# Optimization experiments

Hardware: AMD Instinct MI355X
Metric: run time of the kernel (lower is better)

Reference implementation:

```python
import jax, jax.numpy as jnp
import numpy as np

EPS = 1e-5

def _round_ste(x):
    # straight-through round (identical value in fwd; STE grad in bwd module)
    return x + jax.lax.stop_gradient(jnp.round(x) - x)

def _quant_weight(w, bits):
    # per-tensor symmetric absmax quantization to `bits` bits (BitNet-style)
    qb = float(2 ** (bits - 1) - 1)
    scale = qb / jnp.maximum(jnp.max(jnp.abs(w)), EPS)
    return _round_ste(jnp.clip(w * scale, -qb, qb)) / scale

def _quant_act(x):
    # per-token 8-bit absmax activation quantization
    qb = 127.0
    scale = qb / jnp.maximum(jnp.max(jnp.abs(x), axis=-1, keepdims=True), EPS)
    return _round_ste(jnp.clip(x * scale, -qb, qb)) / scale

def _layernorm(x, gamma, beta):
    mu = jnp.mean(x, axis=-1, keepdims=True)
    var = jnp.mean(jnp.square(x - mu), axis=-1, keepdims=True)
    return (x - mu) * jax.lax.rsqrt(var + EPS) * gamma + beta

def _qlinear(x, w, b, bits):
    return jnp.einsum('btd,fd->btf', _quant_act(x), _quant_weight(w, bits)) + b

def setup_inputs() -> dict:
    key = jax.random.key(0)
    ks = jax.random.split(key, 4)
    B, T, D, F = 8, 2048, 1024, 4096
    return {
        'x': jax.random.normal(ks[0], (B, T, D), dtype=jnp.float32),
        'mask': jnp.ones((B, T, 1), dtype=jnp.float32),
        'ln_gamma': jnp.ones((D,), dtype=jnp.float32),
        'ln_beta': jnp.zeros((D,), dtype=jnp.float32),
        'w1': jax.random.normal(ks[1], (F, D), dtype=jnp.float32) * (1.0 / np.sqrt(D)),
        'b1': jnp.zeros((F,), dtype=jnp.float32),
        'w2': jax.random.normal(ks[2], (D, F), dtype=jnp.float32) * (1.0 / np.sqrt(F)),
        'b2': jnp.zeros((D,), dtype=jnp.float32),
        'bitwidth': 8,
    }

def reference(x, mask, ln_gamma, ln_beta, w1, b1, w2, b2, bitwidth):
    y = _layernorm(x, ln_gamma, ln_beta)           # [B,T,D]
    y = _qlinear(y, w1, b1, bitwidth)              # [B,T,F]
    y = y * jax.nn.sigmoid(y)                      # swish
    y = _qlinear(y, w2, b2, bitwidth)              # [B,T,D]
    seq_mask = mask[:, :, 0][..., None]            # [B,T,1]
    y = y * seq_mask
    return x + 0.5 * y
```

## Files before the change

kernel.cpp:

```cpp
#include <hip/hip_runtime.h>
#include <hip/hip_bf16.h>
#include <stdint.h>


typedef int v4i __attribute__((ext_vector_type(4)));
typedef int v16i __attribute__((ext_vector_type(16)));

__device__ __forceinline__ float wave_max64(float v) {
#pragma unroll
  for (int off = 32; off; off >>= 1) v = fmaxf(v, __shfl_xor(v, off, 64));
  return v;
}

__device__ __forceinline__ void load16_to_lds(const int8_t* g, int8_t* l) {
  __builtin_amdgcn_global_load_lds((const __attribute__((address_space(1))) void*)g,
                                   (__attribute__((address_space(3))) void*)l, 16, 0, 0);
}

__global__ __launch_bounds__(256) void absmax_kernel(const float* __restrict__ w, int n4,
                                                     int* __restrict__ slot) {
  float m = 0.f;
  const float4* w4 = (const float4*)w;
  for (int i = blockIdx.x * 256 + threadIdx.x; i < n4; i += gridDim.x * 256) {
    float4 v = w4[i];
    m = fmaxf(fmaxf(fabsf(v.x), fabsf(v.y)), fmaxf(fmaxf(fabsf(v.z), fabsf(v.w)), m));
  }
  m = wave_max64(m);
  __shared__ float sm[4];
  int lane = threadIdx.x & 63, wv = threadIdx.x >> 6;
  if (!lane) sm[wv] = m;
  __syncthreads();
  if (!threadIdx.x) {
    m = fmaxf(fmaxf(sm[0], sm[1]), fmaxf(sm[2], sm[3]));
    atomicMax(slot, __float_as_int(m));
  }
}

__global__ void scales_kernel(const int* __restrict__ wmax, const int* __restrict__ bits,
                              float* __restrict__ scal) {
  float qb = (float)((1 << (bits[0] - 1)) - 1);
  scal[2] = qb / fmaxf(__int_as_float(wmax[0]), 1e-5f);
  scal[3] = qb / fmaxf(__int_as_float(wmax[1]), 1e-5f);
  scal[4] = qb;
}

__global__ __launch_bounds__(256) void wquant_kernel(const float* __restrict__ w,
                                                     const float* __restrict__ scal, int which,
                                                     int8_t* __restrict__ out) {
  float s = scal[2 + which], qb = scal[4];
  int i = blockIdx.x * 256 + threadIdx.x;
  float4 v = ((const float4*)w)[i];
  char4 q;
  q.x = (char)(int)rintf(fminf(fmaxf(v.x * s, -qb), qb));
  q.y = (char)(int)rintf(fminf(fmaxf(v.y * s, -qb), qb));
  q.z = (char)(int)rintf(fminf(fmaxf(v.z * s, -qb), qb));
  q.w = (char)(int)rintf(fminf(fmaxf(v.w * s, -qb), qb));
  ((char4*)out)[i] = q;
}

__global__ __launch_bounds__(256) void ln_quant_kernel(const float* __restrict__ x,
                                                       const float* __restrict__ gamma,
                                                       const float* __restrict__ beta,
                                                       int8_t* __restrict__ xq,
                                                       float* __restrict__ xscale) {
  const int row = blockIdx.x;
  const int tid = threadIdx.x;
  const float4 v = ((const float4*)(x + (size_t)row * 1024))[tid];
  float s = v.x + v.y + v.z + v.w;
  float ss = fmaf(v.x, v.x, fmaf(v.y, v.y, fmaf(v.z, v.z, v.w * v.w)));
#pragma unroll
  for (int off = 32; off; off >>= 1) {
    s += __shfl_xor(s, off, 64);
    ss += __shfl_xor(ss, off, 64);
  }
  __shared__ float sm[8];
  const int lane = tid & 63, wv = tid >> 6;
  if (!lane) { sm[wv] = s; sm[4 + wv] = ss; }
  __syncthreads();
  s = sm[0] + sm[1] + sm[2] + sm[3];
  ss = sm[4] + sm[5] + sm[6] + sm[7];
  const float mu = s * (1.f / 1024.f);
  const float var = ss * (1.f / 1024.f) - mu * mu;
  const float rstd = rsqrtf(var + 1e-5f);
  const float4 g = ((const float4*)gamma)[tid];
  const float4 bb = ((const float4*)beta)[tid];
  float y0 = (v.x - mu) * rstd * g.x + bb.x;
  float y1 = (v.y - mu) * rstd * g.y + bb.y;
  float y2 = (v.z - mu) * rstd * g.z + bb.z;
  float y3 = (v.w - mu) * rstd * g.w + bb.w;
  float am = fmaxf(fmaxf(fabsf(y0), fabsf(y1)), fmaxf(fabsf(y2), fabsf(y3)));
  am = wave_max64(am);
  __syncthreads();
  if (!lane) sm[wv] = am;
  __syncthreads();
  am = fmaxf(fmaxf(sm[0], sm[1]), fmaxf(sm[2], sm[3]));
  const float scale = 127.f / fmaxf(am, 1e-5f);
  char4 q;
  q.x = (char)(int)rintf(fminf(fmaxf(y0 * scale, -127.f), 127.f));
  q.y = (char)(int)rintf(fminf(fmaxf(y1 * scale, -127.f), 127.f));
  q.z = (char)(int)rintf(fminf(fmaxf(y2 * scale, -127.f), 127.f));
  q.w = (char)(int)rintf(fminf(fmaxf(y3 * scale, -127.f), 127.f));
  ((char4*)(xq + (size_t)row * 1024))[tid] = q;
  if (!tid) xscale[row] = scale;
}

__global__ __launch_bounds__(256) void hquant_kernel(const ushort* __restrict__ h,
                                                     int8_t* __restrict__ hq,
                                                     float* __restrict__ hscale) {
  const int row = blockIdx.x;
  const int tid = threadIdx.x;
  const int4* p = (const int4*)(h + (size_t)row * 4096);
  union { int4 i4; ushort u[8]; } ua, ub;
  ua.i4 = p[tid * 2];
  ub.i4 = p[tid * 2 + 1];
  float f[16];
#pragma unroll
  for (int i = 0; i < 8; ++i) f[i] = __uint_as_float((unsigned)ua.u[i] << 16);
#pragma unroll
  for (int i = 0; i < 8; ++i) f[8 + i] = __uint_as_float((unsigned)ub.u[i] << 16);
  float am = 0.f;
#pragma unroll
  for (int i = 0; i < 16; ++i) am = fmaxf(am, fabsf(f[i]));
  am = wave_max64(am);
  __shared__ float sm[4];
  const int lane = tid & 63, wv = tid >> 6;
  if (!lane) sm[wv] = am;
  __syncthreads();
  am = fmaxf(fmaxf(sm[0], sm[1]), fmaxf(sm[2], sm[3]));
  const float scale = 127.f / fmaxf(am, 1e-5f);
  union { int4 i4; char c[16]; } q;
#pragma unroll
  for (int i = 0; i < 16; ++i)
    q.c[i] = (char)(int)rintf(fminf(fmaxf(f[i] * scale, -127.f), 127.f));
  ((int4*)(hq + (size_t)row * 4096))[tid] = q.i4;
  if (!tid) hscale[row] = scale;
}

template <int K>
__device__ __forceinline__ void gemm_core8(const int8_t* __restrict__ A,
                                           const int8_t* __restrict__ B, int8_t* As, int8_t* Bs,
                                           v16i (&acc)[4][2], int mIdx, int nIdx) {
  const int tid = threadIdx.x;
  const int lane = tid & 63;
  const int wave = tid >> 6;
  const int wm = (wave & 1) * 128;
  const int wn = (wave >> 1) * 64;
  const int lrow = lane & 31;
  const int half = lane >> 5;
  const int x7 = lrow & 7;
  const size_t m0 = (size_t)mIdx * 256;
  const size_t n0 = (size_t)nIdx * 256;

  const int r = tid >> 3;
  const int cs = ((tid & 7) ^ (r & 7)) << 4;
  const int8_t* ga = A + (m0 + r) * K + cs;
  const int8_t* gb = B + (n0 + r) * K + cs;
  int8_t* la = As + tid * 16;
  int8_t* lb = Bs + tid * 16;

  constexpr int NT = K / 128;

#pragma unroll
  for (int p = 0; p < 4; ++p) {
    load16_to_lds(ga + (size_t)(p * 64) * K, la + p * 8192);
    load16_to_lds(gb + (size_t)(p * 64) * K, lb + p * 8192);
  }
  asm volatile("s_waitcnt vmcnt(0)" ::: "memory");
  __builtin_amdgcn_sched_barrier(0);
  __builtin_amdgcn_s_barrier();

  for (int kt = 0; kt < NT; ++kt) {
    const int buf = kt & 1;
    const int8_t* Ab = As + buf * 32768;
    const int8_t* Bb = Bs + buf * 32768;
    int8_t* lan = la + (buf ^ 1) * 32768;
    int8_t* lbn = lb + (buf ^ 1) * 32768;
    const size_t knext = (size_t)(kt + 1) * 128;
    const bool pf = (kt + 1 < NT);
#pragma unroll
    for (int p = 0; p < 4; ++p) {
      if (pf) {
        load16_to_lds(ga + (size_t)(p * 64) * K + knext, lan + p * 8192);
        load16_to_lds(gb + (size_t)(p * 64) * K + knext, lbn + p * 8192);
      }
      const int so = ((p * 2 + half) ^ x7) << 4;
      v4i af[4], bf[2];
#pragma unroll
      for (int i = 0; i < 4; ++i)
        af[i] = *(const v4i*)(Ab + (wm + i * 32 + lrow) * 128 + so);
#pragma unroll
      for (int j = 0; j < 2; ++j)
        bf[j] = *(const v4i*)(Bb + (wn + j * 32 + lrow) * 128 + so);
      __builtin_amdgcn_s_barrier();
      __builtin_amdgcn_s_setprio(1);
#pragma unroll
      for (int i = 0; i < 4; ++i)
#pragma unroll
        for (int j = 0; j < 2; ++j)
          acc[i][j] = __builtin_amdgcn_mfma_i32_32x32x32_i8(af[i], bf[j], acc[i][j], 0, 0, 0);
      __builtin_amdgcn_s_setprio(0);
      if (p == 3) {
        if (pf) asm volatile("s_waitcnt vmcnt(0)" ::: "memory");
        __builtin_amdgcn_sched_barrier(0);
      }
      __builtin_amdgcn_s_barrier();
    }
  }
}

__global__ __launch_bounds__(512, 2) void gemm1_kernel(const int8_t* __restrict__ Aq,
                                                       const int8_t* __restrict__ Bq,
                                                       const float* __restrict__ xscale,
                                                       const float* __restrict__ scal,
                                                       const float* __restrict__ bias,
                                                       ushort* __restrict__ H) {
  __shared__ __align__(16) int8_t As[2 * 256 * 128];
  __shared__ __align__(16) int8_t Bs[2 * 256 * 128];
  const int bid = blockIdx.x;
  const int logical = (bid & 7) * 128 + (bid >> 3);
  const int mIdx = logical >> 4;
  const int nIdx = logical & 15;
  v16i acc[4][2] = {};
  gemm_core8<1024>(Aq, Bq, As, Bs, acc, mIdx, nIdx);
  const float sw1 = scal[2];
  const int lane = threadIdx.x & 63;
  const int wave = threadIdx.x >> 6;
  const int m0 = mIdx * 256 + (wave & 1) * 128;
  const int n0 = nIdx * 256 + (wave >> 1) * 64;
  const int cn = lane & 31;
  const int h4 = (lane >> 5) << 2;
#pragma unroll
  for (int i = 0; i < 4; ++i) {
#pragma unroll
    for (int reg = 0; reg < 16; ++reg) {
      const int row = (reg & 3) + ((reg >> 2) << 3) + h4;
      const int m = m0 + i * 32 + row;
      const float rcp = 1.0f / (xscale[m] * sw1);
#pragma unroll
      for (int j = 0; j < 2; ++j) {
        const int n = n0 + j * 32 + cn;
        const float v = (float)acc[i][j][reg] * rcp + bias[n];
        const float hsw = v / (1.0f + __expf(-v));
        __hip_bfloat16 hb = __float2bfloat16(hsw);
        H[(size_t)m * 4096 + n] = *(const ushort*)&hb;
      }
    }
  }
}

__global__ __launch_bounds__(512, 2) void gemm2_kernel(const int8_t* __restrict__ Aq,
                                                       const int8_t* __restrict__ Bq,
                                                       const float* __restrict__ hscale,
                                                       const float* __restrict__ scal,
                                                       const float* __restrict__ bias,
                                                       const float* __restrict__ x,
                                                       const float* __restrict__ mask,
                                                       float* __restrict__ out) {
  __shared__ __align__(16) int8_t As[2 * 256 * 128];
  __shared__ __align__(16) int8_t Bs[2 * 256 * 128];
  const int bid = blockIdx.x;
  const int logical = (bid & 7) * 32 + (bid >> 3);
  const int mIdx = logical >> 2;
  const int nIdx = logical & 3;
  v16i acc[4][2] = {};
  gemm_core8<4096>(Aq, Bq, As, Bs, acc, mIdx, nIdx);
  const float sw2 = scal[3];
  const int lane = threadIdx.x & 63;
  const int wave = threadIdx.x >> 6;
  const int m0 = mIdx * 256 + (wave & 1) * 128;
  const int n0 = nIdx * 256 + (wave >> 1) * 64;
  const int cn = lane & 31;
  const int h4 = (lane >> 5) << 2;
#pragma unroll
  for (int i = 0; i < 4; ++i) {
#pragma unroll
    for (int reg = 0; reg < 16; ++reg) {
      const int row = (reg & 3) + ((reg >> 2) << 3) + h4;
      const int m = m0 + i * 32 + row;
      const float rcp = 1.0f / (hscale[m] * sw2);
      const float mk = 0.5f * mask[m];
#pragma unroll
      for (int j = 0; j < 2; ++j) {
        const int n = n0 + j * 32 + cn;
        const float v = (float)acc[i][j][reg] * rcp + bias[n];
        const size_t idx = (size_t)m * 1024 + n;
        out[idx] = x[idx] + mk * v;
      }
    }
  }
}

extern "C" void kernel_launch(void* const* d_in, const int* in_sizes, int n_in, void* d_out,
                              int out_size, void* d_ws, size_t ws_size, hipStream_t stream) {
  const float* x = (const float*)d_in[0];
  const float* mask = (const float*)d_in[1];
  const float* gamma = (const float*)d_in[2];
  const float* beta = (const float*)d_in[3];
  const float* w1 = (const float*)d_in[4];
  const float* b1 = (const float*)d_in[5];
  const float* w2 = (const float*)d_in[6];
  const float* b2 = (const float*)d_in[7];
  const int* bits = (const int*)d_in[8];
  float* out = (float*)d_out;

  char* ws = (char*)d_ws;
  int* wmax = (int*)ws;
  float* scal = (float*)ws;
  float* xscale = (float*)(ws + (1u << 20));
  float* hscale = (float*)(ws + (2u << 20));
  int8_t* w1q = (int8_t*)(ws + (4u << 20));
  int8_t* w2q = (int8_t*)(ws + (8u << 20));
  int8_t* xq = (int8_t*)(ws + (12u << 20));
  int8_t* hq = (int8_t*)(ws + (28u << 20));
  ushort* h = (ushort*)(ws + (size_t)(92u << 20));

  const int NW = 4096 * 1024;

  absmax_kernel<<<1024, 256, 0, stream>>>(w1, NW / 4, wmax + 0);
  absmax_kernel<<<1024, 256, 0, stream>>>(w2, NW / 4, wmax + 1);
  scales_kernel<<<1, 1, 0, stream>>>(wmax, bits, scal);
  wquant_kernel<<<NW / 1024, 256, 0, stream>>>(w1, scal, 0, w1q);
  wquant_kernel<<<NW / 1024, 256, 0, stream>>>(w2, scal, 1, w2q);
  ln_quant_kernel<<<16384, 256, 0, stream>>>(x, gamma, beta, xq, xscale);
  gemm1_kernel<<<1024, 512, 0, stream>>>(xq, w1q, xscale, scal, b1, h);
  hquant_kernel<<<16384, 256, 0, stream>>>(h, hq, hscale);
  gemm2_kernel<<<256, 512, 0, stream>>>(hq, w2q, hscale, scal, b2, x, mask, out);
}
```

Baseline: 484.7 us.

## Use 256x128 tiles with triple-buffered LDS pipeline in int8 GEMMs

Replaces the double-buffered 256x256 GEMM core with a 256x128 tile and a three-stage LDS ring, so global loads run two k-tiles ahead under partial vmcnt waits. All four k-substeps' fragments are loaded up front, which cuts the barriers per k-tile from four to two. The grid doubles for both GEMMs, which helps gemm2 (previously only 256 blocks) fill the GPU. The cost is 144KB of LDS per block, which likely caps occupancy at one block per CU, and less reuse per loaded byte.

```diff
diff --git a/kernel.cpp b/kernel.cpp
--- a/kernel.cpp
+++ b/kernel.cpp
@@ -137,75 +137,79 @@
 }
 
 template <int K>
-__device__ __forceinline__ void gemm_core8(const int8_t* __restrict__ A,
-                                           const int8_t* __restrict__ B, int8_t* As, int8_t* Bs,
-                                           v16i (&acc)[4][2], int mIdx, int nIdx) {
+__device__ __forceinline__ void gemm_core_r6(const int8_t* __restrict__ A,
+                                             const int8_t* __restrict__ B, int8_t* smem,
+                                             v16i (&acc)[2][2], int mIdx, int nIdx) {
+  constexpr int NT = K / 128;
   const int tid = threadIdx.x;
   const int lane = tid & 63;
   const int wave = tid >> 6;
-  const int wm = (wave & 1) * 128;
-  const int wn = (wave >> 1) * 64;
+  const int wm = (wave & 3) * 64;
+  const int wn = (wave >> 2) * 64;
   const int lrow = lane & 31;
   const int half = lane >> 5;
   const int x7 = lrow & 7;
   const size_t m0 = (size_t)mIdx * 256;
-  const size_t n0 = (size_t)nIdx * 256;
+  const size_t n0 = (size_t)nIdx * 128;
 
   const int r = tid >> 3;
   const int cs = ((tid & 7) ^ (r & 7)) << 4;
   const int8_t* ga = A + (m0 + r) * K + cs;
   const int8_t* gb = B + (n0 + r) * K + cs;
-  int8_t* la = As + tid * 16;
-  int8_t* lb = Bs + tid * 16;
-
-  constexpr int NT = K / 128;
-
-#pragma unroll
-  for (int p = 0; p < 4; ++p) {
-    load16_to_lds(ga + (size_t)(p * 64) * K, la + p * 8192);
-    load16_to_lds(gb + (size_t)(p * 64) * K, lb + p * 8192);
-  }
+
+  auto stage = [&](int t, int b) {
+    int8_t* la = smem + b * 49152 + tid * 16;
+    int8_t* lb = smem + b * 49152 + 32768 + tid * 16;
+    const size_t ko = (size_t)t * 128;
+#pragma unroll
+    for (int s = 0; s < 4; ++s) load16_to_lds(ga + (size_t)(s * 64) * K + ko, la + s * 8192);
+#pragma unroll
+    for (int s = 0; s < 2; ++s) load16_to_lds(gb + (size_t)(s * 64) * K + ko, lb + s * 8192);
+  };
+
+  auto body = [&](int b) {
+    const int8_t* Ab = smem + b * 49152;
+    const int8_t* Bb = Ab + 32768;
+    __builtin_amdgcn_s_barrier();
+    v4i af[4][2], bf[4][2];
+#pragma unroll
+    for (int ks = 0; ks < 4; ++ks) {
+      const int so = ((ks * 2 + half) ^ x7) << 4;
+#pragma unroll
+      for (int i = 0; i < 2; ++i)
+        af[ks][i] = *(const v4i*)(Ab + (wm + i * 32 + lrow) * 128 + so);
+#pragma unroll
+      for (int j = 0; j < 2; ++j)
+        bf[ks][j] = *(const v4i*)(Bb + (wn + j * 32 + lrow) * 128 + so);
+    }
+    __builtin_amdgcn_s_setprio(1);
+#pragma unroll
+    for (int ks = 0; ks < 4; ++ks)
+#pragma unroll
+      for (int i = 0; i < 2; ++i)
+#pragma unroll
+        for (int j = 0; j < 2; ++j)
+          acc[i][j] =
+              __builtin_amdgcn_mfma_i32_32x32x32_i8(af[ks][i], bf[ks][j], acc[i][j], 0, 0, 0);
+    __builtin_amdgcn_s_setprio(0);
+    __builtin_amdgcn_s_barrier();
+  };
+
+  stage(0, 0);
+  stage(1, 1);
+#pragma unroll 3
+  for (int t = 0; t < NT - 2; ++t) {
+    stage(t + 2, (t + 2) % 3);
+    asm volatile("s_waitcnt vmcnt(12)" ::: "memory");
+    __builtin_amdgcn_sched_barrier(0);
+    body(t % 3);
+  }
+  asm volatile("s_waitcnt vmcnt(6)" ::: "memory");
+  __builtin_amdgcn_sched_barrier(0);
+  body((NT - 2) % 3);
   asm volatile("s_waitcnt vmcnt(0)" ::: "memory");
   __builtin_amdgcn_sched_barrier(0);
-  __builtin_amdgcn_s_barrier();
-
-  for (int kt = 0; kt < NT; ++kt) {
-    const int buf = kt & 1;
-    const int8_t* Ab = As + buf * 32768;
-    const int8_t* Bb = Bs + buf * 32768;
-    int8_t* lan = la + (buf ^ 1) * 32768;
-    int8_t* lbn = lb + (buf ^ 1) * 32768;
-    const size_t knext = (size_t)(kt + 1) * 128;
-    const bool pf = (kt + 1 < NT);
-#pragma unroll
-    for (int p = 0; p < 4; ++p) {
-      if (pf) {
-        load16_to_lds(ga + (size_t)(p * 64) * K + knext, lan + p * 8192);
-        load16_to_lds(gb + (size_t)(p * 64) * K + knext, lbn + p * 8192);
-      }
-      const int so = ((p * 2 + half) ^ x7) << 4;
-      v4i af[4], bf[2];
-#pragma unroll
-      for (int i = 0; i < 4; ++i)
-        af[i] = *(const v4i*)(Ab + (wm + i * 32 + lrow) * 128 + so);
-#pragma unroll
-      for (int j = 0; j < 2; ++j)
-        bf[j] = *(const v4i*)(Bb + (wn + j * 32 + lrow) * 128 + so);
-      __builtin_amdgcn_s_barrier();
-      __builtin_amdgcn_s_setprio(1);
-#pragma unroll
-      for (int i = 0; i < 4; ++i)
-#pragma unroll
-        for (int j = 0; j < 2; ++j)
-          acc[i][j] = __builtin_amdgcn_mfma_i32_32x32x32_i8(af[i], bf[j], acc[i][j], 0, 0, 0);
-      __builtin_amdgcn_s_setprio(0);
-      if (p == 3) {
-        if (pf) asm volatile("s_waitcnt vmcnt(0)" ::: "memory");
-        __builtin_amdgcn_sched_barrier(0);
-      }
-      __builtin_amdgcn_s_barrier();
-    }
-  }
+  body((NT - 1) % 3);
 }
 
 __global__ __launch_bounds__(512, 2) void gemm1_kernel(const int8_t* __restrict__ Aq,
@@ -214,23 +218,22 @@
                                                        const float* __restrict__ scal,
                                                        const float* __restrict__ bias,
                                                        ushort* __restrict__ H) {
-  __shared__ __align__(16) int8_t As[2 * 256 * 128];
-  __shared__ __align__(16) int8_t Bs[2 * 256 * 128];
+  __shared__ __align__(16) int8_t smem[3 * 49152];
   const int bid = blockIdx.x;
-  const int logical = (bid & 7) * 128 + (bid >> 3);
-  const int mIdx = logical >> 4;
-  const int nIdx = logical & 15;
-  v16i acc[4][2] = {};
-  gemm_core8<1024>(Aq, Bq, As, Bs, acc, mIdx, nIdx);
+  const int logical = (bid & 7) * 256 + (bid >> 3);
+  const int mIdx = logical >> 5;
+  const int nIdx = logical & 31;
+  v16i acc[2][2] = {};
+  gemm_core_r6<1024>(Aq, Bq, smem, acc, mIdx, nIdx);
   const float sw1 = scal[2];
   const int lane = threadIdx.x & 63;
   const int wave = threadIdx.x >> 6;
-  const int m0 = mIdx * 256 + (wave & 1) * 128;
-  const int n0 = nIdx * 256 + (wave >> 1) * 64;
+  const int m0 = mIdx * 256 + (wave & 3) * 64;
+  const int n0 = nIdx * 128 + (wave >> 2) * 64;
   const int cn = lane & 31;
   const int h4 = (lane >> 5) << 2;
 #pragma unroll
-  for (int i = 0; i < 4; ++i) {
+  for (int i = 0; i < 2; ++i) {
 #pragma unroll
     for (int reg = 0; reg < 16; ++reg) {
       const int row = (reg & 3) + ((reg >> 2) << 3) + h4;
@@ -256,23 +259,22 @@
                                                        const float* __restrict__ x,
                                                        const float* __restrict__ mask,
                                                        float* __restrict__ out) {
-  __shared__ __align__(16) int8_t As[2 * 256 * 128];
-  __shared__ __align__(16) int8_t Bs[2 * 256 * 128];
+  __shared__ __align__(16) int8_t smem[3 * 49152];
   const int bid = blockIdx.x;
-  const int logical = (bid & 7) * 32 + (bid >> 3);
-  const int mIdx = logical >> 2;
-  const int nIdx = logical & 3;
-  v16i acc[4][2] = {};
-  gemm_core8<4096>(Aq, Bq, As, Bs, acc, mIdx, nIdx);
+  const int logical = (bid & 7) * 64 + (bid >> 3);
+  const int mIdx = logical >> 3;
+  const int nIdx = logical & 7;
+  v16i acc[2][2] = {};
+  gemm_core_r6<4096>(Aq, Bq, smem, acc, mIdx, nIdx);
   const float sw2 = scal[3];
   const int lane = threadIdx.x & 63;
   const int wave = threadIdx.x >> 6;
-  const int m0 = mIdx * 256 + (wave & 1) * 128;
-  const int n0 = nIdx * 256 + (wave >> 1) * 64;
+  const int m0 = mIdx * 256 + (wave & 3) * 64;
+  const int n0 = nIdx * 128 + (wave >> 2) * 64;
   const int cn = lane & 31;
   const int h4 = (lane >> 5) << 2;
 #pragma unroll
-  for (int i = 0; i < 4; ++i) {
+  for (int i = 0; i < 2; ++i) {
 #pragma unroll
     for (int reg = 0; reg < 16; ++reg) {
       const int row = (reg & 3) + ((reg >> 2) << 3) + h4;
@@ -322,7 +324,7 @@
   wquant_kernel<<<NW / 1024, 256, 0, stream>>>(w1, scal, 0, w1q);
   wquant_kernel<<<NW / 1024, 256, 0, stream>>>(w2, scal, 1, w2q);
   ln_quant_kernel<<<16384, 256, 0, stream>>>(x, gamma, beta, xq, xscale);
-  gemm1_kernel<<<1024, 512, 0, stream>>>(xq, w1q, xscale, scal, b1, h);
+  gemm1_kernel<<<2048, 512, 0, stream>>>(xq, w1q, xscale, scal, b1, h);
   hquant_kernel<<<16384, 256, 0, stream>>>(h, hq, hscale);
-  gemm2_kernel<<<256, 512, 0, stream>>>(hq, w2q, hscale, scal, b2, x, mask, out);
-}
+  gemm2_kernel<<<512, 512, 0, stream>>>(hq, w2q, hscale, scal, b2, x, mask, out);
+}
```

New measurement: 455.1 us. 6.1% less time.

## Rewrite int8 GEMM core with 4-stage LDS pipeline and 128x128 wave tiles

Applied to the files above, without the earlier changes.

The int8 GEMM core now uses a 4-buffer LDS ring with a K-step of 64, issuing loads three stages ahead, and double-buffers register fragments so LDS reads for the next step overlap the MFMAs of the current one. Blocks shrink to 256 threads, each wave computing a 128x128 output tile (4x4 MFMA accumulators), which raises register reuse per LDS read. The block-to-tile mapping is also reworked for L2 locality. In exchange occupancy drops to one block per CU with heavy register pressure, which risks spills or less latency hiding.

```diff
diff --git a/kernel.cpp b/kernel.cpp
--- a/kernel.cpp
+++ b/kernel.cpp
@@ -137,96 +137,127 @@
 }
 
 template <int K>
-__device__ __forceinline__ void gemm_core8(const int8_t* __restrict__ A,
-                                           const int8_t* __restrict__ B, int8_t* As, int8_t* Bs,
-                                           v16i (&acc)[4][2], int mIdx, int nIdx) {
+__device__ __forceinline__ void gemm_core_r7(const int8_t* __restrict__ A,
+                                             const int8_t* __restrict__ B, int8_t* smem,
+                                             v16i (&acc)[4][4], int mIdx, int nIdx) {
+  constexpr int NT = K / 64;
   const int tid = threadIdx.x;
   const int lane = tid & 63;
   const int wave = tid >> 6;
   const int wm = (wave & 1) * 128;
-  const int wn = (wave >> 1) * 64;
+  const int wn = (wave >> 1) * 128;
   const int lrow = lane & 31;
   const int half = lane >> 5;
-  const int x7 = lrow & 7;
+  const int sw = (lrow >> 1) & 3;
   const size_t m0 = (size_t)mIdx * 256;
   const size_t n0 = (size_t)nIdx * 256;
 
-  const int r = tid >> 3;
-  const int cs = ((tid & 7) ^ (r & 7)) << 4;
-  const int8_t* ga = A + (m0 + r) * K + cs;
-  const int8_t* gb = B + (n0 + r) * K + cs;
-  int8_t* la = As + tid * 16;
-  int8_t* lb = Bs + tid * 16;
-
-  constexpr int NT = K / 128;
-
-#pragma unroll
-  for (int p = 0; p < 4; ++p) {
-    load16_to_lds(ga + (size_t)(p * 64) * K, la + p * 8192);
-    load16_to_lds(gb + (size_t)(p * 64) * K, lb + p * 8192);
-  }
+  const int r0 = tid >> 2;
+  const int c0 = ((tid & 3) ^ ((tid >> 3) & 3)) << 4;
+  const int8_t* ga = A + (m0 + r0) * K + c0;
+  const int8_t* gb = B + (n0 + r0) * K + c0;
+
+  auto stage = [&](int t) {
+    int8_t* la = smem + (t & 3) * 32768 + tid * 16;
+    const size_t ko = (size_t)t * 64;
+#pragma unroll
+    for (int s = 0; s < 4; ++s)
+      load16_to_lds(ga + (size_t)(s * 64) * K + ko, la + s * 4096);
+#pragma unroll
+    for (int s = 0; s < 4; ++s)
+      load16_to_lds(gb + (size_t)(s * 64) * K + ko, la + 16384 + s * 4096);
+  };
+
+  auto read_frags = [&](int t, v4i (&af)[2][4], v4i (&bf)[2][4]) {
+    const int8_t* Ab = smem + (t & 3) * 32768;
+    const int8_t* Bb = Ab + 16384;
+#pragma unroll
+    for (int ks = 0; ks < 2; ++ks) {
+      const int p = ((ks * 2 + half) ^ sw) << 4;
+#pragma unroll
+      for (int i = 0; i < 4; ++i)
+        af[ks][i] = *(const v4i*)(Ab + (wm + i * 32 + lrow) * 64 + p);
+#pragma unroll
+      for (int j = 0; j < 4; ++j)
+        bf[ks][j] = *(const v4i*)(Bb + (wn + j * 32 + lrow) * 64 + p);
+    }
+  };
+
+  auto mfma_all = [&](v4i (&af)[2][4], v4i (&bf)[2][4]) {
+#pragma unroll
+    for (int ks = 0; ks < 2; ++ks)
+#pragma unroll
+      for (int i = 0; i < 4; ++i)
+#pragma unroll
+        for (int j = 0; j < 4; ++j)
+          acc[i][j] =
+              __builtin_amdgcn_mfma_i32_32x32x32_i8(af[ks][i], bf[ks][j], acc[i][j], 0, 0, 0);
+  };
+
+  v4i a0[2][4], b0[2][4], a1[2][4], b1[2][4];
+
+  stage(0);
+  stage(1);
+  stage(2);
+  asm volatile("s_waitcnt vmcnt(16)" ::: "memory");
+  __builtin_amdgcn_s_barrier();
+  __builtin_amdgcn_sched_barrier(0);
+  read_frags(0, a0, b0);
+
+  for (int t = 0; t < NT - 4; t += 2) {
+    stage(t + 3);
+    asm volatile("s_waitcnt vmcnt(16)" ::: "memory");
+    __builtin_amdgcn_s_barrier();
+    __builtin_amdgcn_sched_barrier(0);
+    read_frags(t + 1, a1, b1);
+    mfma_all(a0, b0);
+    stage(t + 4);
+    asm volatile("s_waitcnt vmcnt(16)" ::: "memory");
+    __builtin_amdgcn_s_barrier();
+    __builtin_amdgcn_sched_barrier(0);
+    read_frags(t + 2, a0, b0);
+    mfma_all(a1, b1);
+  }
+  stage(NT - 1);
+  asm volatile("s_waitcnt vmcnt(16)" ::: "memory");
+  __builtin_amdgcn_s_barrier();
+  __builtin_amdgcn_sched_barrier(0);
+  read_frags(NT - 3, a1, b1);
+  mfma_all(a0, b0);
+
+  asm volatile("s_waitcnt vmcnt(8)" ::: "memory");
+  __builtin_amdgcn_s_barrier();
+  __builtin_amdgcn_sched_barrier(0);
+  read_frags(NT - 2, a0, b0);
+  mfma_all(a1, b1);
+
   asm volatile("s_waitcnt vmcnt(0)" ::: "memory");
+  __builtin_amdgcn_s_barrier();
   __builtin_amdgcn_sched_barrier(0);
-  __builtin_amdgcn_s_barrier();
-
-  for (int kt = 0; kt < NT; ++kt) {
-    const int buf = kt & 1;
-    const int8_t* Ab = As + buf * 32768;
-    const int8_t* Bb = Bs + buf * 32768;
-    int8_t* lan = la + (buf ^ 1) * 32768;
-    int8_t* lbn = lb + (buf ^ 1) * 32768;
-    const size_t knext = (size_t)(kt + 1) * 128;
-    const bool pf = (kt + 1 < NT);
-#pragma unroll
-    for (int p = 0; p < 4; ++p) {
-      if (pf) {
-        load16_to_lds(ga + (size_t)(p * 64) * K + knext, lan + p * 8192);
-        load16_to_lds(gb + (size_t)(p * 64) * K + knext, lbn + p * 8192);
-      }
-      const int so = ((p * 2 + half) ^ x7) << 4;
-      v4i af[4], bf[2];
-#pragma unroll
-      for (int i = 0; i < 4; ++i)
-        af[i] = *(const v4i*)(Ab + (wm + i * 32 + lrow) * 128 + so);
-#pragma unroll
-      for (int j = 0; j < 2; ++j)
-        bf[j] = *(const v4i*)(Bb + (wn + j * 32 + lrow) * 128 + so);
-      __builtin_amdgcn_s_barrier();
-      __builtin_amdgcn_s_setprio(1);
-#pragma unroll
-      for (int i = 0; i < 4; ++i)
-#pragma unroll
-        for (int j = 0; j < 2; ++j)
-          acc[i][j] = __builtin_amdgcn_mfma_i32_32x32x32_i8(af[i], bf[j], acc[i][j], 0, 0, 0);
-      __builtin_amdgcn_s_setprio(0);
-      if (p == 3) {
-        if (pf) asm volatile("s_waitcnt vmcnt(0)" ::: "memory");
-        __builtin_amdgcn_sched_barrier(0);
-      }
-      __builtin_amdgcn_s_barrier();
-    }
-  }
-}
-
-__global__ __launch_bounds__(512, 2) void gemm1_kernel(const int8_t* __restrict__ Aq,
+  read_frags(NT - 1, a1, b1);
+  mfma_all(a0, b0);
+
+  mfma_all(a1, b1);
+}
+
+__global__ __launch_bounds__(256, 1) void gemm1_kernel(const int8_t* __restrict__ Aq,
                                                        const int8_t* __restrict__ Bq,
                                                        const float* __restrict__ xscale,
                                                        const float* __restrict__ scal,
                                                        const float* __restrict__ bias,
                                                        ushort* __restrict__ H) {
-  __shared__ __align__(16) int8_t As[2 * 256 * 128];
-  __shared__ __align__(16) int8_t Bs[2 * 256 * 128];
+  __shared__ __align__(16) int8_t smem[4 * 32768];
   const int bid = blockIdx.x;
-  const int logical = (bid & 7) * 128 + (bid >> 3);
-  const int mIdx = logical >> 4;
-  const int nIdx = logical & 15;
-  v16i acc[4][2] = {};
-  gemm_core8<1024>(Aq, Bq, As, Bs, acc, mIdx, nIdx);
+  const int loc = bid >> 3;
+  const int nIdx = loc & 15;
+  const int mIdx = (bid & 7) * 8 + (loc >> 4);
+  v16i acc[4][4] = {};
+  gemm_core_r7<1024>(Aq, Bq, smem, acc, mIdx, nIdx);
   const float sw1 = scal[2];
   const int lane = threadIdx.x & 63;
   const int wave = threadIdx.x >> 6;
   const int m0 = mIdx * 256 + (wave & 1) * 128;
-  const int n0 = nIdx * 256 + (wave >> 1) * 64;
+  const int n0 = nIdx * 256 + (wave >> 1) * 128;
   const int cn = lane & 31;
   const int h4 = (lane >> 5) << 2;
 #pragma unroll
@@ -237,7 +268,7 @@
       const int m = m0 + i * 32 + row;
       const float rcp = 1.0f / (xscale[m] * sw1);
 #pragma unroll
-      for (int j = 0; j < 2; ++j) {
+      for (int j = 0; j < 4; ++j) {
         const int n = n0 + j * 32 + cn;
         const float v = (float)acc[i][j][reg] * rcp + bias[n];
         const float hsw = v / (1.0f + __expf(-v));
@@ -248,7 +279,7 @@
   }
 }
 
-__global__ __launch_bounds__(512, 2) void gemm2_kernel(const int8_t* __restrict__ Aq,
+__global__ __launch_bounds__(256, 1) void gemm2_kernel(const int8_t* __restrict__ Aq,
                                                        const int8_t* __restrict__ Bq,
                                                        const float* __restrict__ hscale,
                                                        const float* __restrict__ scal,
@@ -256,19 +287,18 @@
                                                        const float* __restrict__ x,
                                                        const float* __restrict__ mask,
                                                        float* __restrict__ out) {
-  __shared__ __align__(16) int8_t As[2 * 256 * 128];
-  __shared__ __align__(16) int8_t Bs[2 * 256 * 128];
+  __shared__ __align__(16) int8_t smem[4 * 32768];
   const int bid = blockIdx.x;
-  const int logical = (bid & 7) * 32 + (bid >> 3);
-  const int mIdx = logical >> 2;
-  const int nIdx = logical & 3;
-  v16i acc[4][2] = {};
-  gemm_core8<4096>(Aq, Bq, As, Bs, acc, mIdx, nIdx);
+  const int loc = bid >> 3;
+  const int nIdx = loc & 3;
+  const int mIdx = (bid & 7) * 8 + (loc >> 2);
+  v16i acc[4][4] = {};
+  gemm_core_r7<4096>(Aq, Bq, smem, acc, mIdx, nIdx);
   const float sw2 = scal[3];
   const int lane = threadIdx.x & 63;
   const int wave = threadIdx.x >> 6;
   const int m0 = mIdx * 256 + (wave & 1) * 128;
-  const int n0 = nIdx * 256 + (wave >> 1) * 64;
+  const int n0 = nIdx * 256 + (wave >> 1) * 128;
   const int cn = lane & 31;
   const int h4 = (lane >> 5) << 2;
 #pragma unroll
@@ -280,7 +310,7 @@
       const float rcp = 1.0f / (hscale[m] * sw2);
       const float mk = 0.5f * mask[m];
 #pragma unroll
-      for (int j = 0; j < 2; ++j) {
+      for (int j = 0; j < 4; ++j) {
         const int n = n0 + j * 32 + cn;
         const float v = (float)acc[i][j][reg] * rcp + bias[n];
         const size_t idx = (size_t)m * 1024 + n;
@@ -322,7 +352,7 @@
   wquant_kernel<<<NW / 1024, 256, 0, stream>>>(w1, scal, 0, w1q);
   wquant_kernel<<<NW / 1024, 256, 0, stream>>>(w2, scal, 1, w2q);
   ln_quant_kernel<<<16384, 256, 0, stream>>>(x, gamma, beta, xq, xscale);
-  gemm1_kernel<<<1024, 512, 0, stream>>>(xq, w1q, xscale, scal, b1, h);
+  gemm1_kernel<<<1024, 256, 0, stream>>>(xq, w1q, xscale, scal, b1, h);
   hquant_kernel<<<16384, 256, 0, stream>>>(h, hq, hscale);
-  gemm2_kernel<<<256, 512, 0, stream>>>(hq, w2q, hscale, scal, b2, x, mask, out);
-}
+  gemm2_kernel<<<256, 256, 0, stream>>>(hq, w2q, hscale, scal, b2, x, mask, out);
+}
```

After: 421.7 us. 13.0% less time.

## Restructure int8 GEMM core into fine-grained ping-pong pipeline with register-reused quads

Applied to the files above, without the earlier changes.

Replaces the per-128-K double-buffered GEMM loop with a two-buffer schedule that stages loads in half-tiles interleaved between four MFMA quadrants. Fragments are held in registers and reused across quadrant pairs, so fewer LDS reads are issued per MFMA and global loads overlap with compute at finer granularity. Block-to-tile mapping is also changed so each XCD group gets contiguous M rows. The cost is more barriers per iteration and higher register pressure from holding 16 fragment vectors.

```diff
diff --git a/kernel.cpp b/kernel.cpp
--- a/kernel.cpp
+++ b/kernel.cpp
@@ -137,9 +137,10 @@
 }
 
 template <int K>
-__device__ __forceinline__ void gemm_core8(const int8_t* __restrict__ A,
-                                           const int8_t* __restrict__ B, int8_t* As, int8_t* Bs,
-                                           v16i (&acc)[4][2], int mIdx, int nIdx) {
+__device__ __forceinline__ void gemm_core_r8(const int8_t* __restrict__ A,
+                                             const int8_t* __restrict__ B, int8_t* smem,
+                                             v16i (&acc)[4][2], int mIdx, int nIdx) {
+  constexpr int NI = K / 256;
   const int tid = threadIdx.x;
   const int lane = tid & 63;
   const int wave = tid >> 6;
@@ -151,60 +152,118 @@
   const size_t m0 = (size_t)mIdx * 256;
   const size_t n0 = (size_t)nIdx * 256;
 
-  const int r = tid >> 3;
-  const int cs = ((tid & 7) ^ (r & 7)) << 4;
-  const int8_t* ga = A + (m0 + r) * K + cs;
-  const int8_t* gb = B + (n0 + r) * K + cs;
-  int8_t* la = As + tid * 16;
-  int8_t* lb = Bs + tid * 16;
-
-  constexpr int NT = K / 128;
-
-#pragma unroll
-  for (int p = 0; p < 4; ++p) {
-    load16_to_lds(ga + (size_t)(p * 64) * K, la + p * 8192);
-    load16_to_lds(gb + (size_t)(p * 64) * K, lb + p * 8192);
-  }
-  asm volatile("s_waitcnt vmcnt(0)" ::: "memory");
+  const int r0 = tid >> 3;
+  const int c0 = ((tid & 7) ^ (r0 & 7)) << 4;
+  const int8_t* ga = A + (m0 + r0) * K + c0;
+  const int8_t* gb = B + (n0 + r0) * K + c0;
+  int8_t* const lds0 = smem;
+  int8_t* const lds1 = smem + 65536;
+
+  auto stgHalf = [&](size_t ko, int8_t* lb, int h) {
+    const int s0 = h * 2;
+#pragma unroll
+    for (int s = s0; s < s0 + 2; ++s) {
+      load16_to_lds(ga + (size_t)(s * 64) * K + ko, lb + s * 8192 + tid * 16);
+      load16_to_lds(gb + (size_t)(s * 64) * K + ko, lb + 32768 + s * 8192 + tid * 16);
+    }
+  };
+
+  auto rdA = [&](const int8_t* lb, int i, int ks) {
+    return *(const v4i*)(lb + (wm + i * 32 + lrow) * 128 + (((ks * 2 + half) ^ x7) << 4));
+  };
+  auto rdB = [&](const int8_t* lb, int j, int ks) {
+    return *(const v4i*)(lb + 32768 + (wn + j * 32 + lrow) * 128 + (((ks * 2 + half) ^ x7) << 4));
+  };
+
+  v4i aR[2][4], bR[2][4];
+
+  auto quad = [&](int mh, int nh) {
+    __builtin_amdgcn_s_setprio(1);
+#pragma unroll
+    for (int ks = 0; ks < 4; ++ks) {
+      acc[2 * mh + 0][nh] = __builtin_amdgcn_mfma_i32_32x32x32_i8(aR[0][ks], bR[nh][ks],
+                                                                  acc[2 * mh + 0][nh], 0, 0, 0);
+      acc[2 * mh + 1][nh] = __builtin_amdgcn_mfma_i32_32x32x32_i8(aR[1][ks], bR[nh][ks],
+                                                                  acc[2 * mh + 1][nh], 0, 0, 0);
+    }
+    __builtin_amdgcn_s_setprio(0);
+  };
+
+  stgHalf(0, lds0, 0);
+  stgHalf(0, lds0, 1);
+  stgHalf(128, lds1, 0);
+  asm volatile("s_waitcnt vmcnt(4)" ::: "memory");
   __builtin_amdgcn_sched_barrier(0);
   __builtin_amdgcn_s_barrier();
 
-  for (int kt = 0; kt < NT; ++kt) {
-    const int buf = kt & 1;
-    const int8_t* Ab = As + buf * 32768;
-    const int8_t* Bb = Bs + buf * 32768;
-    int8_t* lan = la + (buf ^ 1) * 32768;
-    int8_t* lbn = lb + (buf ^ 1) * 32768;
-    const size_t knext = (size_t)(kt + 1) * 128;
-    const bool pf = (kt + 1 < NT);
-#pragma unroll
-    for (int p = 0; p < 4; ++p) {
-      if (pf) {
-        load16_to_lds(ga + (size_t)(p * 64) * K + knext, lan + p * 8192);
-        load16_to_lds(gb + (size_t)(p * 64) * K + knext, lbn + p * 8192);
-      }
-      const int so = ((p * 2 + half) ^ x7) << 4;
-      v4i af[4], bf[2];
-#pragma unroll
-      for (int i = 0; i < 4; ++i)
-        af[i] = *(const v4i*)(Ab + (wm + i * 32 + lrow) * 128 + so);
-#pragma unroll
-      for (int j = 0; j < 2; ++j)
-        bf[j] = *(const v4i*)(Bb + (wn + j * 32 + lrow) * 128 + so);
-      __builtin_amdgcn_s_barrier();
-      __builtin_amdgcn_s_setprio(1);
-#pragma unroll
-      for (int i = 0; i < 4; ++i)
-#pragma unroll
-        for (int j = 0; j < 2; ++j)
-          acc[i][j] = __builtin_amdgcn_mfma_i32_32x32x32_i8(af[i], bf[j], acc[i][j], 0, 0, 0);
-      __builtin_amdgcn_s_setprio(0);
-      if (p == 3) {
-        if (pf) asm volatile("s_waitcnt vmcnt(0)" ::: "memory");
-        __builtin_amdgcn_sched_barrier(0);
-      }
-      __builtin_amdgcn_s_barrier();
-    }
+#pragma unroll 1
+  for (int it = 0; it < NI; ++it) {
+    const bool nl = (it < NI - 1);
+    const size_t ko = (size_t)it * 256;
+#pragma unroll
+    for (int ks = 0; ks < 4; ++ks) {
+      aR[0][ks] = rdA(lds0, 0, ks);
+      aR[1][ks] = rdA(lds0, 1, ks);
+      bR[0][ks] = rdB(lds0, 0, ks);
+    }
+    stgHalf(ko + 128, lds1, 1);
+    __builtin_amdgcn_s_barrier();
+    quad(0, 0);
+    __builtin_amdgcn_s_barrier();
+#pragma unroll
+    for (int ks = 0; ks < 4; ++ks) bR[1][ks] = rdB(lds0, 1, ks);
+    __builtin_amdgcn_s_barrier();
+    quad(0, 1);
+    __builtin_amdgcn_s_barrier();
+#pragma unroll
+    for (int ks = 0; ks < 4; ++ks) {
+      aR[0][ks] = rdA(lds0, 2, ks);
+      aR[1][ks] = rdA(lds0, 3, ks);
+    }
+    __builtin_amdgcn_s_barrier();
+    quad(1, 0);
+    __builtin_amdgcn_s_barrier();
+    if (nl) stgHalf(ko + 256, lds0, 0);
+    __builtin_amdgcn_s_barrier();
+    quad(1, 1);
+    if (nl) {
+      asm volatile("s_waitcnt vmcnt(4)" ::: "memory");
+    } else {
+      asm volatile("s_waitcnt vmcnt(0)" ::: "memory");
+    }
+    __builtin_amdgcn_sched_barrier(0);
+    __builtin_amdgcn_s_barrier();
+#pragma unroll
+    for (int ks = 0; ks < 4; ++ks) {
+      aR[0][ks] = rdA(lds1, 0, ks);
+      aR[1][ks] = rdA(lds1, 1, ks);
+      bR[0][ks] = rdB(lds1, 0, ks);
+    }
+    if (nl) stgHalf(ko + 256, lds0, 1);
+    __builtin_amdgcn_s_barrier();
+    quad(0, 0);
+    __builtin_amdgcn_s_barrier();
+#pragma unroll
+    for (int ks = 0; ks < 4; ++ks) bR[1][ks] = rdB(lds1, 1, ks);
+    __builtin_amdgcn_s_barrier();
+    quad(0, 1);
+    __builtin_amdgcn_s_barrier();
+#pragma unroll
+    for (int ks = 0; ks < 4; ++ks) {
+      aR[0][ks] = rdA(lds1, 2, ks);
+      aR[1][ks] = rdA(lds1, 3, ks);
+    }
+    __builtin_amdgcn_s_barrier();
+    quad(1, 0);
+    __builtin_amdgcn_s_barrier();
+    if (nl) stgHalf(ko + 384, lds1, 0);
+    __builtin_amdgcn_s_barrier();
+    quad(1, 1);
+    if (nl) {
+      asm volatile("s_waitcnt vmcnt(4)" ::: "memory");
+      __builtin_amdgcn_sched_barrier(0);
+    }
+    __builtin_amdgcn_s_barrier();
   }
 }
 
@@ -214,14 +273,13 @@
                                                        const float* __restrict__ scal,
                                                        const float* __restrict__ bias,
                                                        ushort* __restrict__ H) {
-  __shared__ __align__(16) int8_t As[2 * 256 * 128];
-  __shared__ __align__(16) int8_t Bs[2 * 256 * 128];
+  __shared__ __align__(16) int8_t smem[2 * 65536];
   const int bid = blockIdx.x;
-  const int logical = (bid & 7) * 128 + (bid >> 3);
-  const int mIdx = logical >> 4;
-  const int nIdx = logical & 15;
+  const int loc = bid >> 3;
+  const int nIdx = loc & 15;
+  const int mIdx = (bid & 7) * 8 + (loc >> 4);
   v16i acc[4][2] = {};
-  gemm_core8<1024>(Aq, Bq, As, Bs, acc, mIdx, nIdx);
+  gemm_core_r8<1024>(Aq, Bq, smem, acc, mIdx, nIdx);
   const float sw1 = scal[2];
   const int lane = threadIdx.x & 63;
   const int wave = threadIdx.x >> 6;
@@ -256,14 +314,13 @@
                                                        const float* __restrict__ x,
                                                        const float* __restrict__ mask,
                                                        float* __restrict__ out) {
-  __shared__ __align__(16) int8_t As[2 * 256 * 128];
-  __shared__ __align__(16) int8_t Bs[2 * 256 * 128];
+  __shared__ __align__(16) int8_t smem[2 * 65536];
   const int bid = blockIdx.x;
-  const int logical = (bid & 7) * 32 + (bid >> 3);
-  const int mIdx = logical >> 2;
-  const int nIdx = logical & 3;
+  const int loc = bid >> 3;
+  const int nIdx = loc & 3;
+  const int mIdx = (bid & 7) * 8 + (loc >> 2);
   v16i acc[4][2] = {};
-  gemm_core8<4096>(Aq, Bq, As, Bs, acc, mIdx, nIdx);
+  gemm_core_r8<4096>(Aq, Bq, smem, acc, mIdx, nIdx);
   const float sw2 = scal[3];
   const int lane = threadIdx.x & 63;
   const int wave = threadIdx.x >> 6;
```

Result: faster. 427.4 us (-11.8%).
